# Optimization experiments

Hardware: AMD Instinct MI355X
Metric: run time of the kernel (lower is better)

The kernel has to match this reference:

```python
import jax, jax.numpy as jnp
import numpy as np

N_NODES = 100000
N_EDGES = 800000
IN_FEAT = 128


def setup_inputs() -> dict:
    key = jax.random.key(0)
    k_feat, k_src, k_dst, k_w1, k_b1, k_w2 = jax.random.split(key, 6)
    feature = jax.random.normal(k_feat, (N_NODES, IN_FEAT), dtype=jnp.float32)
    src = jax.random.randint(k_src, (N_EDGES,), 0, N_NODES, dtype=jnp.int64)
    dst = jax.random.randint(k_dst, (N_EDGES,), 0, N_NODES, dtype=jnp.int64)
    # nn.Linear params: y = x @ W.T + b; Kaiming-uniform-ish init scale
    lim1 = 1.0 / np.sqrt(2 * IN_FEAT)
    W1 = jax.random.uniform(k_w1, (IN_FEAT, 2 * IN_FEAT), jnp.float32, -lim1, lim1)
    b1 = jax.random.uniform(k_b1, (IN_FEAT,), jnp.float32, -lim1, lim1)
    lim2 = 1.0 / np.sqrt(IN_FEAT)
    W2 = jax.random.uniform(k_w2, (1, IN_FEAT), jnp.float32, -lim2, lim2)
    b2 = jnp.zeros((1,), jnp.float32)
    return {"feature": feature, "src": src, "dst": dst,
            "W1": W1, "b1": b1, "W2": W2, "b2": b2}


def reference(feature, src, dst, W1, b1, W2, b2):
    # gather src/dst node feats and concat -> [E, 2*in_feat]
    h = jnp.concatenate([feature[src], feature[dst]], axis=1)
    # 2-layer MLP per edge: Linear -> ReLU -> Linear
    hid = jax.nn.relu(h @ W1.T + b1)            # [E, in_feat]
    score = hid @ W2.T + b2                      # [E, 1]
    return score
```

## Files before the change

kernel.cpp:

```cpp
#include <hip/hip_runtime.h>
#include <stdint.h>

typedef short short8 __attribute__((ext_vector_type(8)));
typedef float floatx4 __attribute__((ext_vector_type(4)));

#define NN 100000
#define NE 800000
#define KF 128
#define PC 256
#define BM 64
#define LDK 136

__device__ __forceinline__ unsigned short f2bf(float x) {
  union { float f; unsigned u; } c; c.f = x;
  unsigned u = c.u + 0x7FFFu + ((c.u >> 16) & 1u);
  return (unsigned short)(u >> 16);
}
__device__ __forceinline__ float bfl(unsigned u) {
  union { unsigned u; float f; } c; c.u = u << 16; return c.f;
}
__device__ __forceinline__ float bfh(unsigned u) {
  union { unsigned u; float f; } c; c.u = u & 0xFFFF0000u; return c.f;
}

extern "C" __global__ void __launch_bounds__(256)
node_proj_kernel(const float* __restrict__ feature,
                 const float* __restrict__ W1,
                 const float* __restrict__ b1,
                 unsigned short* __restrict__ P)
{
  __shared__ unsigned short Wl[128 * LDK];
  __shared__ unsigned short Al[BM * LDK];
  __shared__ float b1l[128];

  const int t = threadIdx.x;
  const int nodeBase = blockIdx.x * BM;

  #pragma unroll
  for (int it = 0; it < 4; ++it) {
    int c  = t + it * 256;
    int nl = c >> 4;
    int kc = (c & 15) << 3;
    int node = nodeBase + nl;
    float4 f0 = make_float4(0.f, 0.f, 0.f, 0.f);
    float4 f1 = make_float4(0.f, 0.f, 0.f, 0.f);
    if (node < NN) {
      const float* fp = feature + (size_t)node * KF + kc;
      f0 = ((const float4*)fp)[0];
      f1 = ((const float4*)fp)[1];
    }
    short8 v;
    v[0] = (short)f2bf(f0.x); v[1] = (short)f2bf(f0.y);
    v[2] = (short)f2bf(f0.z); v[3] = (short)f2bf(f0.w);
    v[4] = (short)f2bf(f1.x); v[5] = (short)f2bf(f1.y);
    v[6] = (short)f2bf(f1.z); v[7] = (short)f2bf(f1.w);
    *(short8*)&Al[nl * LDK + kc] = v;
  }
  if (t < 128) b1l[t] = b1[t];

  const int wave = t >> 6;
  const int lane = t & 63;
  const int m16  = lane & 15;
  const int quad = lane >> 4;

  short8 a0, a1, a2, a3;
  bool aLoaded = false;

  for (int half = 0; half < 2; ++half) {
    #pragma unroll
    for (int it = 0; it < 8; ++it) {
      int c  = t + it * 256;
      int jl = c >> 4;
      int kc = (c & 15) << 3;
      const float* sp = W1 + jl * 256 + half * 128 + kc;
      float4 f0 = ((const float4*)sp)[0];
      float4 f1 = ((const float4*)sp)[1];
      short8 v;
      v[0] = (short)f2bf(f0.x); v[1] = (short)f2bf(f0.y);
      v[2] = (short)f2bf(f0.z); v[3] = (short)f2bf(f0.w);
      v[4] = (short)f2bf(f1.x); v[5] = (short)f2bf(f1.y);
      v[6] = (short)f2bf(f1.z); v[7] = (short)f2bf(f1.w);
      *(short8*)&Wl[jl * LDK + kc] = v;
    }
    __syncthreads();

    if (!aLoaded) {
      const unsigned short* arow = &Al[(wave * 16 + m16) * LDK + quad * 8];
      a0 = *(const short8*)(arow + 0);
      a1 = *(const short8*)(arow + 32);
      a2 = *(const short8*)(arow + 64);
      a3 = *(const short8*)(arow + 96);
      aLoaded = true;
    }

    #pragma unroll
    for (int nt = 0; nt < 8; ++nt) {
      floatx4 acc = {0.f, 0.f, 0.f, 0.f};
      const unsigned short* wrow = &Wl[(nt * 16 + m16) * LDK + quad * 8];
      acc = __builtin_amdgcn_mfma_f32_16x16x32_bf16(a0, *(const short8*)(wrow +  0), acc, 0, 0, 0);
      acc = __builtin_amdgcn_mfma_f32_16x16x32_bf16(a1, *(const short8*)(wrow + 32), acc, 0, 0, 0);
      acc = __builtin_amdgcn_mfma_f32_16x16x32_bf16(a2, *(const short8*)(wrow + 64), acc, 0, 0, 0);
      acc = __builtin_amdgcn_mfma_f32_16x16x32_bf16(a3, *(const short8*)(wrow + 96), acc, 0, 0, 0);

      int n = half * 128 + nt * 16 + m16;
      float bias = (half == 0) ? b1l[nt * 16 + m16] : 0.f;
      #pragma unroll
      for (int r = 0; r < 4; ++r) {
        int node = nodeBase + wave * 16 + quad * 4 + r;
        if (node < NN) P[(size_t)node * PC + n] = f2bf(acc[r] + bias);
      }
    }
    __syncthreads();
  }
}

extern "C" __global__ void __launch_bounds__(256)
edge_score_kernel(const unsigned short* __restrict__ P,
                  const int* __restrict__ src,
                  const int* __restrict__ dst,
                  const float* __restrict__ W2,
                  const float* __restrict__ b2,
                  float* __restrict__ out)
{
  const int t    = threadIdx.x;
  const int lane = t & 15;
  const int g    = t >> 4;
  const int e    = blockIdx.x * 16 + g;
  if (e >= NE) return;

  const int s = src[e];
  const int d = dst[e];

  const uint4 u1 = *(const uint4*)(P + (size_t)s * PC + lane * 8);
  const uint4 u2 = *(const uint4*)(P + (size_t)d * PC + 128 + lane * 8);
  const float4 wA = *(const float4*)(W2 + lane * 8);
  const float4 wB = *(const float4*)(W2 + lane * 8 + 4);

  float acc = 0.f;
  {
    float x0 = bfl(u1.x) + bfl(u2.x); x0 = fmaxf(x0, 0.f); acc += x0 * wA.x;
    float x1 = bfh(u1.x) + bfh(u2.x); x1 = fmaxf(x1, 0.f); acc += x1 * wA.y;
  }
  {
    float x0 = bfl(u1.y) + bfl(u2.y); x0 = fmaxf(x0, 0.f); acc += x0 * wA.z;
    float x1 = bfh(u1.y) + bfh(u2.y); x1 = fmaxf(x1, 0.f); acc += x1 * wA.w;
  }
  {
    float x0 = bfl(u1.z) + bfl(u2.z); x0 = fmaxf(x0, 0.f); acc += x0 * wB.x;
    float x1 = bfh(u1.z) + bfh(u2.z); x1 = fmaxf(x1, 0.f); acc += x1 * wB.y;
  }
  {
    float x0 = bfl(u1.w) + bfl(u2.w); x0 = fmaxf(x0, 0.f); acc += x0 * wB.z;
    float x1 = bfh(u1.w) + bfh(u2.w); x1 = fmaxf(x1, 0.f); acc += x1 * wB.w;
  }

  acc += __shfl_xor(acc, 8);
  acc += __shfl_xor(acc, 4);
  acc += __shfl_xor(acc, 2);
  acc += __shfl_xor(acc, 1);

  if (lane == 0) out[e] = acc + b2[0];
}

extern "C" void kernel_launch(void* const* d_in, const int* in_sizes, int n_in,
                              void* d_out, int out_size, void* d_ws, size_t ws_size,
                              hipStream_t stream)
{
  const float* feature = (const float*)d_in[0];
  const int*   src     = (const int*)d_in[1];
  const int*   dst     = (const int*)d_in[2];
  const float* W1      = (const float*)d_in[3];
  const float* b1      = (const float*)d_in[4];
  const float* W2      = (const float*)d_in[5];
  const float* b2      = (const float*)d_in[6];
  float* out = (float*)d_out;
  unsigned short* P = (unsigned short*)d_ws;

  dim3 grid1((NN + BM - 1) / BM);
  node_proj_kernel<<<grid1, 256, 0, stream>>>(feature, W1, b1, P);

  dim3 grid2((NE + 15) / 16);
  edge_score_kernel<<<grid2, 256, 0, stream>>>(P, src, dst, W2, b2, out);
}
```

Measured before the change: 170.2 us.

## Keep W1 fragments in registers with persistent node loop; widen edge gather per thread

The node projection kernel becomes persistent (768 blocks): each wave loads its 64-column slice of the bf16 W1 once into registers, then loops over 32-node tiles staged through LDS. This removes the repeated per-block W1 conversion and LDS staging. The edge kernel now uses 4 lanes per edge and processes two edges per thread with wider contiguous loads and fewer shuffles, so more memory requests are in flight per thread. Bounds checks are dropped, which relies on NN being divisible by 32 and NE by 128; register pressure rises with the held fragments.

New measurement: 208.2 us. 22.3% more time.

```diff
diff --git a/kernel.cpp b/kernel.cpp
--- a/kernel.cpp
+++ b/kernel.cpp
@@ -8,8 +8,7 @@
 #define NE 800000
 #define KF 128
 #define PC 256
-#define BM 64
-#define LDK 136
+#define LDA 136
 
 __device__ __forceinline__ unsigned short f2bf(float x) {
   union { float f; unsigned u; } c; c.f = x;
@@ -23,56 +22,30 @@
   union { unsigned u; float f; } c; c.u = u & 0xFFFF0000u; return c.f;
 }
 
-extern "C" __global__ void __launch_bounds__(256)
+extern "C" __global__ void __launch_bounds__(256, 3)
 node_proj_kernel(const float* __restrict__ feature,
                  const float* __restrict__ W1,
                  const float* __restrict__ b1,
                  unsigned short* __restrict__ P)
 {
-  __shared__ unsigned short Wl[128 * LDK];
-  __shared__ unsigned short Al[BM * LDK];
-  __shared__ float b1l[128];
-
-  const int t = threadIdx.x;
-  const int nodeBase = blockIdx.x * BM;
-
-  #pragma unroll
-  for (int it = 0; it < 4; ++it) {
-    int c  = t + it * 256;
-    int nl = c >> 4;
-    int kc = (c & 15) << 3;
-    int node = nodeBase + nl;
-    float4 f0 = make_float4(0.f, 0.f, 0.f, 0.f);
-    float4 f1 = make_float4(0.f, 0.f, 0.f, 0.f);
-    if (node < NN) {
-      const float* fp = feature + (size_t)node * KF + kc;
-      f0 = ((const float4*)fp)[0];
-      f1 = ((const float4*)fp)[1];
-    }
-    short8 v;
-    v[0] = (short)f2bf(f0.x); v[1] = (short)f2bf(f0.y);
-    v[2] = (short)f2bf(f0.z); v[3] = (short)f2bf(f0.w);
-    v[4] = (short)f2bf(f1.x); v[5] = (short)f2bf(f1.y);
-    v[6] = (short)f2bf(f1.z); v[7] = (short)f2bf(f1.w);
-    *(short8*)&Al[nl * LDK + kc] = v;
-  }
-  if (t < 128) b1l[t] = b1[t];
-
-  const int wave = t >> 6;
+  __shared__ unsigned short Al[32 * LDA];
+
+  const int t    = threadIdx.x;
+  const int w    = t >> 6;
   const int lane = t & 63;
   const int m16  = lane & 15;
   const int quad = lane >> 4;
-
-  short8 a0, a1, a2, a3;
-  bool aLoaded = false;
-
-  for (int half = 0; half < 2; ++half) {
-    #pragma unroll
-    for (int it = 0; it < 8; ++it) {
-      int c  = t + it * 256;
-      int jl = c >> 4;
-      int kc = (c & 15) << 3;
-      const float* sp = W1 + jl * 256 + half * 128 + kc;
+  const int colBase = w * 64;
+
+  short8 bfrag[4][4];
+  #pragma unroll
+  for (int ct = 0; ct < 4; ++ct) {
+    const int n = colBase + ct * 16 + m16;
+    const int j = n & 127;
+    const int koff = (n >> 7) * 128;
+    #pragma unroll
+    for (int kc = 0; kc < 4; ++kc) {
+      const float* sp = W1 + j * 256 + koff + kc * 32 + quad * 8;
       float4 f0 = ((const float4*)sp)[0];
       float4 f1 = ((const float4*)sp)[1];
       short8 v;
@@ -80,38 +53,84 @@
       v[2] = (short)f2bf(f0.z); v[3] = (short)f2bf(f0.w);
       v[4] = (short)f2bf(f1.x); v[5] = (short)f2bf(f1.y);
       v[6] = (short)f2bf(f1.z); v[7] = (short)f2bf(f1.w);
-      *(short8*)&Wl[jl * LDK + kc] = v;
+      bfrag[ct][kc] = v;
+    }
+  }
+
+  float bias[4];
+  #pragma unroll
+  for (int ct = 0; ct < 4; ++ct)
+    bias[ct] = (w < 2) ? b1[colBase + ct * 16 + m16] : 0.f;
+
+  for (int base = blockIdx.x * 32; base < NN; base += gridDim.x * 32) {
+    #pragma unroll
+    for (int it = 0; it < 2; ++it) {
+      int c   = t + it * 256;
+      int nl  = c >> 4;
+      int kc8 = (c & 15) << 3;
+      const float* fp = feature + (size_t)(base + nl) * KF + kc8;
+      float4 f0 = ((const float4*)fp)[0];
+      float4 f1 = ((const float4*)fp)[1];
+      short8 v;
+      v[0] = (short)f2bf(f0.x); v[1] = (short)f2bf(f0.y);
+      v[2] = (short)f2bf(f0.z); v[3] = (short)f2bf(f0.w);
+      v[4] = (short)f2bf(f1.x); v[5] = (short)f2bf(f1.y);
+      v[6] = (short)f2bf(f1.z); v[7] = (short)f2bf(f1.w);
+      *(short8*)&Al[nl * LDA + kc8] = v;
     }
     __syncthreads();
 
-    if (!aLoaded) {
-      const unsigned short* arow = &Al[(wave * 16 + m16) * LDK + quad * 8];
-      a0 = *(const short8*)(arow + 0);
-      a1 = *(const short8*)(arow + 32);
-      a2 = *(const short8*)(arow + 64);
-      a3 = *(const short8*)(arow + 96);
-      aLoaded = true;
+    short8 afrag[2][4];
+    #pragma unroll
+    for (int rt = 0; rt < 2; ++rt) {
+      const unsigned short* ar = &Al[(rt * 16 + m16) * LDA + quad * 8];
+      #pragma unroll
+      for (int kc = 0; kc < 4; ++kc)
+        afrag[rt][kc] = *(const short8*)(ar + kc * 32);
     }
 
-    #pragma unroll
-    for (int nt = 0; nt < 8; ++nt) {
-      floatx4 acc = {0.f, 0.f, 0.f, 0.f};
-      const unsigned short* wrow = &Wl[(nt * 16 + m16) * LDK + quad * 8];
-      acc = __builtin_amdgcn_mfma_f32_16x16x32_bf16(a0, *(const short8*)(wrow +  0), acc, 0, 0, 0);
-      acc = __builtin_amdgcn_mfma_f32_16x16x32_bf16(a1, *(const short8*)(wrow + 32), acc, 0, 0, 0);
-      acc = __builtin_amdgcn_mfma_f32_16x16x32_bf16(a2, *(const short8*)(wrow + 64), acc, 0, 0, 0);
-      acc = __builtin_amdgcn_mfma_f32_16x16x32_bf16(a3, *(const short8*)(wrow + 96), acc, 0, 0, 0);
-
-      int n = half * 128 + nt * 16 + m16;
-      float bias = (half == 0) ? b1l[nt * 16 + m16] : 0.f;
-      #pragma unroll
-      for (int r = 0; r < 4; ++r) {
-        int node = nodeBase + wave * 16 + quad * 4 + r;
-        if (node < NN) P[(size_t)node * PC + n] = f2bf(acc[r] + bias);
+    floatx4 acc[2][4];
+    #pragma unroll
+    for (int rt = 0; rt < 2; ++rt)
+      #pragma unroll
+      for (int ct = 0; ct < 4; ++ct)
+        acc[rt][ct] = (floatx4){0.f, 0.f, 0.f, 0.f};
+
+    #pragma unroll
+    for (int kc = 0; kc < 4; ++kc)
+      #pragma unroll
+      for (int rt = 0; rt < 2; ++rt)
+        #pragma unroll
+        for (int ct = 0; ct < 4; ++ct)
+          acc[rt][ct] = __builtin_amdgcn_mfma_f32_16x16x32_bf16(
+              afrag[rt][kc], bfrag[ct][kc], acc[rt][ct], 0, 0, 0);
+
+    #pragma unroll
+    for (int rt = 0; rt < 2; ++rt)
+      #pragma unroll
+      for (int ct = 0; ct < 4; ++ct) {
+        const int col = colBase + ct * 16 + m16;
+        #pragma unroll
+        for (int r = 0; r < 4; ++r) {
+          const int node = base + rt * 16 + quad * 4 + r;
+          P[(size_t)node * PC + col] = f2bf(acc[rt][ct][r] + bias[ct]);
+        }
       }
-    }
     __syncthreads();
   }
+}
+
+__device__ __forceinline__ float dot8(uint4 u1, uint4 u2, float4 wA, float4 wB) {
+  float a = 0.f;
+  a += fmaxf(bfl(u1.x) + bfl(u2.x), 0.f) * wA.x;
+  a += fmaxf(bfh(u1.x) + bfh(u2.x), 0.f) * wA.y;
+  a += fmaxf(bfl(u1.y) + bfl(u2.y), 0.f) * wA.z;
+  a += fmaxf(bfh(u1.y) + bfh(u2.y), 0.f) * wA.w;
+  a += fmaxf(bfl(u1.z) + bfl(u2.z), 0.f) * wB.x;
+  a += fmaxf(bfh(u1.z) + bfh(u2.z), 0.f) * wB.y;
+  a += fmaxf(bfl(u1.w) + bfl(u2.w), 0.f) * wB.z;
+  a += fmaxf(bfh(u1.w) + bfh(u2.w), 0.f) * wB.w;
+  return a;
 }
 
 extern "C" __global__ void __launch_bounds__(256)
@@ -122,44 +141,44 @@
                   const float* __restrict__ b2,
                   float* __restrict__ out)
 {
-  const int t    = threadIdx.x;
-  const int lane = t & 15;
-  const int g    = t >> 4;
-  const int e    = blockIdx.x * 16 + g;
-  if (e >= NE) return;
-
-  const int s = src[e];
-  const int d = dst[e];
-
-  const uint4 u1 = *(const uint4*)(P + (size_t)s * PC + lane * 8);
-  const uint4 u2 = *(const uint4*)(P + (size_t)d * PC + 128 + lane * 8);
-  const float4 wA = *(const float4*)(W2 + lane * 8);
-  const float4 wB = *(const float4*)(W2 + lane * 8 + 4);
-
-  float acc = 0.f;
-  {
-    float x0 = bfl(u1.x) + bfl(u2.x); x0 = fmaxf(x0, 0.f); acc += x0 * wA.x;
-    float x1 = bfh(u1.x) + bfh(u2.x); x1 = fmaxf(x1, 0.f); acc += x1 * wA.y;
+  const int t  = threadIdx.x;
+  const int l4 = t & 3;
+  const int g  = t >> 2;
+  const int e0 = blockIdx.x * 128 + g;
+  const int e1 = e0 + 64;
+
+  const int s0 = src[e0], d0 = dst[e0];
+  const int s1 = src[e1], d1 = dst[e1];
+
+  const uint4* p1a = (const uint4*)(P + (size_t)s0 * PC + l4 * 32);
+  const uint4* p2a = (const uint4*)(P + (size_t)d0 * PC + 128 + l4 * 32);
+  const uint4* p1b = (const uint4*)(P + (size_t)s1 * PC + l4 * 32);
+  const uint4* p2b = (const uint4*)(P + (size_t)d1 * PC + 128 + l4 * 32);
+
+  uint4 a0 = p1a[0], a1 = p1a[1], a2 = p1a[2], a3 = p1a[3];
+  uint4 b0 = p2a[0], b1v = p2a[1], b2v = p2a[2], b3 = p2a[3];
+  uint4 c0 = p1b[0], c1 = p1b[1], c2 = p1b[2], c3 = p1b[3];
+  uint4 e0v = p2b[0], e1v = p2b[1], e2v = p2b[2], e3 = p2b[3];
+
+  const float4* wp = (const float4*)(W2 + l4 * 32);
+  float4 w0 = wp[0], w1 = wp[1], w2 = wp[2], w3 = wp[3];
+  float4 w4 = wp[4], w5 = wp[5], w6 = wp[6], w7 = wp[7];
+
+  float accA = dot8(a0, b0, w0, w1) + dot8(a1, b1v, w2, w3)
+             + dot8(a2, b2v, w4, w5) + dot8(a3, b3, w6, w7);
+  float accB = dot8(c0, e0v, w0, w1) + dot8(c1, e1v, w2, w3)
+             + dot8(c2, e2v, w4, w5) + dot8(c3, e3, w6, w7);
+
+  accA += __shfl_xor(accA, 2);
+  accA += __shfl_xor(accA, 1);
+  accB += __shfl_xor(accB, 2);
+  accB += __shfl_xor(accB, 1);
+
+  if (l4 == 0) {
+    const float bb = b2[0];
+    out[e0] = accA + bb;
+    out[e1] = accB + bb;
   }
-  {
-    float x0 = bfl(u1.y) + bfl(u2.y); x0 = fmaxf(x0, 0.f); acc += x0 * wA.z;
-    float x1 = bfh(u1.y) + bfh(u2.y); x1 = fmaxf(x1, 0.f); acc += x1 * wA.w;
-  }
-  {
-    float x0 = bfl(u1.z) + bfl(u2.z); x0 = fmaxf(x0, 0.f); acc += x0 * wB.x;
-    float x1 = bfh(u1.z) + bfh(u2.z); x1 = fmaxf(x1, 0.f); acc += x1 * wB.y;
-  }
-  {
-    float x0 = bfl(u1.w) + bfl(u2.w); x0 = fmaxf(x0, 0.f); acc += x0 * wB.z;
-    float x1 = bfh(u1.w) + bfh(u2.w); x1 = fmaxf(x1, 0.f); acc += x1 * wB.w;
-  }
-
-  acc += __shfl_xor(acc, 8);
-  acc += __shfl_xor(acc, 4);
-  acc += __shfl_xor(acc, 2);
-  acc += __shfl_xor(acc, 1);
-
-  if (lane == 0) out[e] = acc + b2[0];
 }
 
 extern "C" void kernel_launch(void* const* d_in, const int* in_sizes, int n_in,
@@ -176,9 +195,6 @@
   float* out = (float*)d_out;
   unsigned short* P = (unsigned short*)d_ws;
 
-  dim3 grid1((NN + BM - 1) / BM);
-  node_proj_kernel<<<grid1, 256, 0, stream>>>(feature, W1, b1, P);
-
-  dim3 grid2((NE + 15) / 16);
-  edge_score_kernel<<<grid2, 256, 0, stream>>>(P, src, dst, W2, b2, out);
-}
+  node_proj_kernel<<<768, 256, 0, stream>>>(feature, W1, b1, P);
+  edge_score_kernel<<<NE / 128, 256, 0, stream>>>(P, src, dst, W2, b2, out);
+}
```
